# Optimization experiments

Hardware: AMD Instinct MI355X
Metric: run time of the kernel (lower is better)

Reference implementation:

```python
import jax, jax.numpy as jnp
import numpy as np

NEG_SLOPE = 0.01  # torch leaky_relu default

def _lrelu(x):
    return jax.nn.leaky_relu(x, NEG_SLOPE)

def _l2norm(x, axis):
    # torch F.normalize(p=2, eps=1e-12)
    n = jnp.linalg.norm(x, axis=axis, keepdims=True)
    return x / jnp.maximum(n, 1e-12)

def setup_inputs() -> dict:
    key = jax.random.key(0)
    ks = jax.random.split(key, 12)
    Nda, Nq, C, Din, Dout = 10000, 64, 1024, 128, 256
    target_adj = (jax.random.uniform(ks[0], (Nda, Nda)) < 0.002).astype(jnp.float32)
    query_adj = (jax.random.uniform(ks[1], (Nq, Nq)) < 0.2).astype(jnp.float32)
    node_features_da = jax.random.normal(ks[2], (Nda, Din), dtype=jnp.float32)
    node_features_q = jax.random.normal(ks[3], (Nq, Din), dtype=jnp.float32)
    candidate_set = jax.random.randint(ks[4], (C,), 0, Nda)
    candidate_adj = (jax.random.uniform(ks[5], (C, C)) < 0.01).astype(jnp.float32)
    s_in = 1.0 / np.sqrt(Din).astype(np.float32)
    s_out = 1.0 / np.sqrt(Dout).astype(np.float32)
    W1_da = jax.random.normal(ks[6], (Din, Dout), dtype=jnp.float32) * s_in
    W1_q = jax.random.normal(ks[7], (Din, Dout), dtype=jnp.float32) * s_in
    W2_da = jax.random.normal(ks[8], (Dout, Dout), dtype=jnp.float32) * s_out
    W2_q = jax.random.normal(ks[9], (Dout, Dout), dtype=jnp.float32) * s_out
    threshold = jnp.float32(0.2)
    return {"target_adj": target_adj, "node_features_da": node_features_da,
            "query_adj": query_adj, "node_features_q": node_features_q,
            "candidate_set": candidate_set, "candidate_adj": candidate_adj,
            "threshold": threshold, "W1_da": W1_da, "W1_q": W1_q,
            "W2_da": W2_da, "W2_q": W2_q}

def _cross_cosine(q, da, candidate_set):
    # cosine similarity between each query node and each candidate target node: [Nq, C]
    return _l2norm(q, 1) @ _l2norm(da[candidate_set], 1).T

def reference(target_adj, node_features_da, query_adj, node_features_q,
              candidate_set, candidate_adj, threshold, W1_da, W1_q, W2_da, W2_q):
    # layer 1: GCN propagation on both graphs (gcn(adj,x) = adj @ x @ W)
    da1 = _lrelu(target_adj @ (node_features_da @ W1_da))   # [Nda, D]
    q1 = _lrelu(query_adj @ (node_features_q @ W1_q))       # [Nq, D]
    c1 = _cross_cosine(q1, da1, candidate_set)               # [Nq, C]
    pre_da1 = da1[candidate_set]                             # [C, D]
    # NOTE: da1[candidate_set].data = ... mutates a temporary in torch -> no-op on da1
    att_da1 = _lrelu(da1)                                    # dropout in eval = identity
    h1_q = c1 @ pre_da1                                      # [Nq, D]
    att_q1 = _lrelu(q1 + _l2norm(h1_q, 0))
    # layer 2
    da2 = _lrelu(target_adj @ (att_da1 @ W2_da))
    q2 = _lrelu(query_adj @ (att_q1 @ W2_q))
    c2 = _cross_cosine(q2, da2, candidate_set)
    pre_da2 = da2[candidate_set]
    att_da2 = _lrelu(da2)                                    # in-place update is again a no-op
    h2_q = c2 @ pre_da2
    att_q2 = _lrelu(q2 + _l2norm(h2_q, 0))
    # graph-level matching score per target node
    emb = jnp.mean(att_q2, axis=0, keepdims=True)            # [1, D]
    num = att_da2 @ emb[0]                                   # [Nda]
    den = jnp.maximum(jnp.linalg.norm(att_da2, axis=1) * jnp.linalg.norm(emb), 1e-8)
    end = (num / den)[None, :]                               # [1, Nda]
    # threshold selection expressed with a mask (jit-safe, same math: excluded
    # rows/cols are zero and do not affect L2 norms, sums, or the trace)
    m = (end[0] > threshold).astype(att_da2.dtype)           # [Nda]
    F_ = att_da2 * m[:, None]
    re_adj = F_ @ F_.T                                       # [Nda, Nda]
    nor_re = _l2norm(re_adj, 1) * target_adj                 # elementwise with original adj
    cnt = jnp.sum(m)
    total = jnp.sum(nor_re)
    tr = jnp.trace(nor_re)
    has = cnt > 0
    pre_avg_degree = jnp.where(has, total / jnp.maximum(cnt, 1.0), 0.0)
    pre_avg_nodes = jnp.where(has, tr, 0.0)
    pre_density = jnp.where(has, 2.0 * total / (tr * (tr - 1.0) + 1e-4), 0.0)
    return (end, att_da2, att_q2, pre_avg_degree, pre_density, pre_avg_nodes)
```

## Files before the change

kernel.cpp:

```cpp
#include <hip/hip_runtime.h>

constexpr int NDA = 10000;
constexpr int NQ  = 64;
constexpr int CND = 1024;
constexpr int DIN = 128;
constexpr int D   = 256;
constexpr int CAP = 96;
constexpr int NB_BIG = ((NDA + 63) / 64) * (D / 64);

#define LRELU(x) ((x) >= 0.f ? (x) : 0.01f * (x))

__device__ __forceinline__ float wave_red64(float v) {
#pragma unroll
    for (int o = 32; o; o >>= 1) v += __shfl_down(v, o);
    return v;
}

struct GemmSmem { float As[32][68]; float Bs[32][68]; };

template <bool RELU_A, bool RELU_C>
__device__ __forceinline__ void gemm_body(GemmSmem& sm, int bx, int by,
                                          const float* __restrict__ A,
                                          const float* __restrict__ B,
                                          float* __restrict__ C,
                                          int M, int N, int K) {
    const int bm = bx * 64, bn = by * 64;
    const int tid = threadIdx.x;
    const int tx = tid & 15, ty = tid >> 4;
    const int lm = tid >> 2, lk = (tid & 3) * 8;
    const int kb = tid >> 3, nb = (tid & 7) * 8;
    const bool aValid = (bm + lm) < M;
    const float* aPtr = A + (size_t)(bm + lm) * K + lk;
    const float* bPtr = B + (size_t)kb * N + bn + nb;
    float4 ra0 = make_float4(0.f, 0.f, 0.f, 0.f), ra1 = ra0, rb0, rb1;
    if (aValid) { ra0 = *(const float4*)aPtr; ra1 = *(const float4*)(aPtr + 4); }
    rb0 = *(const float4*)bPtr;
    rb1 = *(const float4*)(bPtr + 4);
    float acc[4][4] = {};
    for (int k0 = 0; k0 < K; k0 += 32) {
        float4 wa0 = ra0, wa1 = ra1, wb0 = rb0, wb1 = rb1;
        if (RELU_A) {
            wa0.x = LRELU(wa0.x); wa0.y = LRELU(wa0.y); wa0.z = LRELU(wa0.z); wa0.w = LRELU(wa0.w);
            wa1.x = LRELU(wa1.x); wa1.y = LRELU(wa1.y); wa1.z = LRELU(wa1.z); wa1.w = LRELU(wa1.w);
        }
        sm.As[lk + 0][lm] = wa0.x; sm.As[lk + 1][lm] = wa0.y;
        sm.As[lk + 2][lm] = wa0.z; sm.As[lk + 3][lm] = wa0.w;
        sm.As[lk + 4][lm] = wa1.x; sm.As[lk + 5][lm] = wa1.y;
        sm.As[lk + 6][lm] = wa1.z; sm.As[lk + 7][lm] = wa1.w;
        *(float4*)&sm.Bs[kb][nb]     = wb0;
        *(float4*)&sm.Bs[kb][nb + 4] = wb1;
        __syncthreads();
        if (k0 + 32 < K) {
            if (aValid) {
                ra0 = *(const float4*)(aPtr + k0 + 32);
                ra1 = *(const float4*)(aPtr + k0 + 36);
            }
            rb0 = *(const float4*)(bPtr + (size_t)(k0 + 32) * N);
            rb1 = *(const float4*)(bPtr + (size_t)(k0 + 32) * N + 4);
        }
#pragma unroll
        for (int kk = 0; kk < 32; kk++) {
            float av[4], bv[4];
#pragma unroll
            for (int i = 0; i < 4; i++) av[i] = sm.As[kk][ty * 4 + i];
#pragma unroll
            for (int j = 0; j < 4; j++) bv[j] = sm.Bs[kk][tx * 4 + j];
#pragma unroll
            for (int i = 0; i < 4; i++)
#pragma unroll
                for (int j = 0; j < 4; j++) acc[i][j] += av[i] * bv[j];
        }
        __syncthreads();
    }
#pragma unroll
    for (int i = 0; i < 4; i++) {
        int r = bm + ty * 4 + i;
        if (r < M) {
            float4 v = make_float4(acc[i][0], acc[i][1], acc[i][2], acc[i][3]);
            if (RELU_C) { v.x = LRELU(v.x); v.y = LRELU(v.y); v.z = LRELU(v.z); v.w = LRELU(v.w); }
            *(float4*)(C + (size_t)r * N + bn + tx * 4) = v;
        }
    }
}

__device__ __forceinline__ void csr_body(const float* __restrict__ adj,
                                         int* __restrict__ cols,
                                         int* __restrict__ rowcnt, int row) {
    __shared__ int scnt;
    if (threadIdx.x == 0) scnt = 0;
    __syncthreads();
    const float4* rp = (const float4*)(adj + (size_t)row * NDA);
    for (int i = threadIdx.x; i < NDA / 4; i += 256) {
        float4 v = rp[i];
        if (v.x != 0.f) { int s = atomicAdd(&scnt, 1); if (s < CAP) cols[row * CAP + s] = 4 * i; }
        if (v.y != 0.f) { int s = atomicAdd(&scnt, 1); if (s < CAP) cols[row * CAP + s] = 4 * i + 1; }
        if (v.z != 0.f) { int s = atomicAdd(&scnt, 1); if (s < CAP) cols[row * CAP + s] = 4 * i + 2; }
        if (v.w != 0.f) { int s = atomicAdd(&scnt, 1); if (s < CAP) cols[row * CAP + s] = 4 * i + 3; }
    }
    __syncthreads();
    if (threadIdx.x == 0) rowcnt[row] = min(scnt, CAP);
}

__device__ __forceinline__ void spmm_body(const int* __restrict__ cols,
                                          const int* __restrict__ rowcnt,
                                          const float* __restrict__ X,
                                          float* __restrict__ out1,
                                          float* __restrict__ out2, int row) {
    int d = threadIdx.x;
    int cnt = rowcnt[row];
    __shared__ int sc[CAP];
    if (d < cnt) sc[d] = cols[row * CAP + d];
    __syncthreads();
    float a0 = 0.f, a1 = 0.f, a2 = 0.f, a3 = 0.f;
    int k = 0;
    for (; k + 4 <= cnt; k += 4) {
        a0 += X[(size_t)sc[k + 0] * D + d];
        a1 += X[(size_t)sc[k + 1] * D + d];
        a2 += X[(size_t)sc[k + 2] * D + d];
        a3 += X[(size_t)sc[k + 3] * D + d];
    }
    for (; k < cnt; k++) a0 += X[(size_t)sc[k] * D + d];
    float v = LRELU(a0 + a1 + a2 + a3);
    out1[(size_t)row * D + d] = v;
    if (out2) out2[(size_t)row * D + d] = LRELU(v);
}

__device__ __forceinline__ void cross_body(const float* __restrict__ q,
                                           const float* __restrict__ da,
                                           const int* __restrict__ cand,
                                           float* __restrict__ hpart,
                                           int r, int qr) {
    __shared__ float qs[D];
    __shared__ float cmw[256];
    __shared__ int sci[256];
    __shared__ float red[4];
    __shared__ float sqn;
    int d = threadIdx.x;
    float qv = q[r * D + d];
    qs[d] = qv;
    sci[d] = cand[qr * 256 + d];
    float p = wave_red64(qv * qv);
    int w = d >> 6, lane = d & 63;
    if (lane == 0) red[w] = p;
    __syncthreads();
    if (d == 0) sqn = fmaxf(sqrtf(red[0] + red[1] + red[2] + red[3]), 1e-12f);
    __syncthreads();
    float qn = sqn;
    {
        const float4* ap = (const float4*)(da + (size_t)sci[d] * D);
        float dot = 0.f, sq = 0.f;
#pragma unroll 8
        for (int k = 0; k < D / 4; k++) {
            float4 v = ap[k];
            dot += qs[4 * k] * v.x + qs[4 * k + 1] * v.y + qs[4 * k + 2] * v.z + qs[4 * k + 3] * v.w;
            sq  += v.x * v.x + v.y * v.y + v.z * v.z + v.w * v.w;
        }
        cmw[d] = dot / (qn * fmaxf(sqrtf(sq), 1e-12f));
    }
    __syncthreads();
    float a0 = 0.f, a1 = 0.f, a2 = 0.f, a3 = 0.f, a4 = 0.f, a5 = 0.f, a6 = 0.f, a7 = 0.f;
    for (int c = 0; c < 256; c += 8) {
        a0 += cmw[c + 0] * da[(size_t)sci[c + 0] * D + d];
        a1 += cmw[c + 1] * da[(size_t)sci[c + 1] * D + d];
        a2 += cmw[c + 2] * da[(size_t)sci[c + 2] * D + d];
        a3 += cmw[c + 3] * da[(size_t)sci[c + 3] * D + d];
        a4 += cmw[c + 4] * da[(size_t)sci[c + 4] * D + d];
        a5 += cmw[c + 5] * da[(size_t)sci[c + 5] * D + d];
        a6 += cmw[c + 6] * da[(size_t)sci[c + 6] * D + d];
        a7 += cmw[c + 7] * da[(size_t)sci[c + 7] * D + d];
    }
    hpart[((size_t)qr * NQ + r) * D + d] = ((a0 + a1) + (a2 + a3)) + ((a4 + a5) + (a6 + a7));
}

__global__ __launch_bounds__(256) void stage0_kernel(const float* __restrict__ adj,
                                                     int* __restrict__ cols,
                                                     int* __restrict__ rowcnt,
                                                     const float* __restrict__ Fda,
                                                     const float* __restrict__ W1da,
                                                     float* __restrict__ X1,
                                                     const float* __restrict__ Fq,
                                                     const float* __restrict__ W1q,
                                                     float* __restrict__ Xq) {
    __shared__ GemmSmem gs;
    int bid = blockIdx.x;
    if (bid < NB_BIG) {
        gemm_body<false, false>(gs, bid >> 2, bid & 3, Fda, W1da, X1, NDA, D, DIN);
    } else if (bid < NB_BIG + 4) {
        gemm_body<false, false>(gs, 0, bid - NB_BIG, Fq, W1q, Xq, NQ, D, DIN);
    } else {
        csr_body(adj, cols, rowcnt, bid - (NB_BIG + 4));
    }
}

__global__ __launch_bounds__(256) void stage_sg_kernel(const int* __restrict__ cols,
                                                       const int* __restrict__ rowcnt,
                                                       const float* __restrict__ X,
                                                       float* __restrict__ out1,
                                                       float* __restrict__ out2,
                                                       const float* __restrict__ Aq,
                                                       const float* __restrict__ Bq,
                                                       float* __restrict__ Cq) {
    __shared__ GemmSmem gs;
    int bid = blockIdx.x;
    if (bid < 4) {
        gemm_body<false, true>(gs, 0, bid, Aq, Bq, Cq, NQ, D, NQ);
    } else {
        spmm_body(cols, rowcnt, X, out1, out2, bid - 4);
    }
}

__global__ __launch_bounds__(256) void mergeA_kernel(const float* __restrict__ q1,
                                                     const float* __restrict__ da1,
                                                     const int* __restrict__ cand,
                                                     float* __restrict__ hpart,
                                                     const float* __restrict__ W2da,
                                                     float* __restrict__ Y2) {
    int bid = blockIdx.x;
    if (bid < 256) {
        cross_body(q1, da1, cand, hpart, bid >> 2, bid & 3);
    } else {
        __shared__ GemmSmem gs;
        int b = bid - 256;
        gemm_body<true, false>(gs, b >> 2, b & 3, da1, W2da, Y2, NDA, D, D);
    }
}

__global__ __launch_bounds__(256) void cross_kernel(const float* __restrict__ q,
                                                    const float* __restrict__ da,
                                                    const int* __restrict__ cand,
                                                    float* __restrict__ hpart) {
    cross_body(q, da, cand, hpart, blockIdx.x, blockIdx.y);
}

__global__ __launch_bounds__(256) void qfused_kernel(const float* __restrict__ q,
                                                     const float* __restrict__ hpart,
                                                     const float* __restrict__ W2q,
                                                     float* __restrict__ Zq) {
    __shared__ float aqT[D][68];
    __shared__ float Bs[32][68];
    int d = threadIdx.x;
    float hv[NQ];
    float ss = 0.f;
#pragma unroll
    for (int r = 0; r < NQ; r++) {
        float h = hpart[(size_t)r * D + d]
                + hpart[(size_t)(NQ + r) * D + d]
                + hpart[(size_t)(2 * NQ + r) * D + d]
                + hpart[(size_t)(3 * NQ + r) * D + d];
        hv[r] = h;
        ss += h * h;
    }
    float inv = 1.f / fmaxf(sqrtf(ss), 1e-12f);
#pragma unroll
    for (int r = 0; r < NQ; r++) {
        float v = q[r * D + d] + hv[r] * inv;
        aqT[d][r] = LRELU(v);
    }
    __syncthreads();
    const int bn = blockIdx.x * 64;
    const int tx = d & 15, ty = d >> 4;
    const int kb = d >> 3, nb = (d & 7) * 8;
    float acc[4][4] = {};
    for (int k0 = 0; k0 < D; k0 += 32) {
        float4 b0 = *(const float4*)(W2q + (size_t)(k0 + kb) * D + bn + nb);
        float4 b1 = *(const float4*)(W2q + (size_t)(k0 + kb) * D + bn + nb + 4);
        *(float4*)&Bs[kb][nb]     = b0;
        *(float4*)&Bs[kb][nb + 4] = b1;
        __syncthreads();
#pragma unroll
        for (int kk = 0; kk < 32; kk++) {
            float av[4], bv[4];
#pragma unroll
            for (int i = 0; i < 4; i++) av[i] = aqT[k0 + kk][ty * 4 + i];
#pragma unroll
            for (int j = 0; j < 4; j++) bv[j] = Bs[kk][tx * 4 + j];
#pragma unroll
            for (int i = 0; i < 4; i++)
#pragma unroll
                for (int j = 0; j < 4; j++) acc[i][j] += av[i] * bv[j];
        }
        __syncthreads();
    }
#pragma unroll
    for (int i = 0; i < 4; i++) {
        float4 v = make_float4(acc[i][0], acc[i][1], acc[i][2], acc[i][3]);
        *(float4*)(Zq + (size_t)(ty * 4 + i) * D + bn + tx * 4) = v;
    }
}

__global__ __launch_bounds__(256) void attq_kernel(const float* __restrict__ q,
                                                   const float* __restrict__ hpart,
                                                   float* __restrict__ attq,
                                                   float* __restrict__ emb) {
    int d = threadIdx.x;
    float hv[NQ];
    float ss = 0.f;
#pragma unroll
    for (int r = 0; r < NQ; r++) {
        float h = hpart[(size_t)r * D + d]
                + hpart[(size_t)(NQ + r) * D + d]
                + hpart[(size_t)(2 * NQ + r) * D + d]
                + hpart[(size_t)(3 * NQ + r) * D + d];
        hv[r] = h;
        ss += h * h;
    }
    float inv = 1.f / fmaxf(sqrtf(ss), 1e-12f);
    float es = 0.f;
#pragma unroll
    for (int r = 0; r < NQ; r++) {
        float v = q[r * D + d] + hv[r] * inv;
        v = LRELU(v);
        attq[r * D + d] = v;
        es += v;
    }
    if (emb) {
        float e = es * (1.f / (float)NQ);
        emb[d] = e;
        float p = wave_red64(e * e);
        __shared__ float red[4];
        int w = d >> 6, lane = d & 63;
        if (lane == 0) red[w] = p;
        __syncthreads();
        if (d == 0) emb[D] = sqrtf(red[0] + red[1] + red[2] + red[3]);
    }
}

__global__ __launch_bounds__(256) void end_kernel(const float* __restrict__ A,
                                                  const float* __restrict__ emb,
                                                  const float* __restrict__ thr_p,
                                                  float* __restrict__ endv,
                                                  float* __restrict__ m,
                                                  float* __restrict__ cnt) {
    __shared__ float se[D];
    __shared__ float scnt;
    int d = threadIdx.x;
    se[d] = emb[d];
    if (d == 0) scnt = 0.f;
    __syncthreads();
    float embn = emb[D];
    float thr = *thr_p;
    int w = d >> 6, lane = d & 63;
    int row = blockIdx.x * 4 + w;
    const float* ar = A + (size_t)row * D;
    float num = 0.f, sq = 0.f;
#pragma unroll
    for (int s = 0; s < 4; s++) {
        float v = ar[lane + 64 * s];
        num += v * se[lane + 64 * s];
        sq += v * v;
    }
#pragma unroll
    for (int o = 32; o; o >>= 1) { num += __shfl_down(num, o); sq += __shfl_down(sq, o); }
    if (lane == 0) {
        float den = fmaxf(sqrtf(sq) * embn, 1e-8f);
        float e = num / den;
        endv[row] = e;
        float mv = e > thr ? 1.f : 0.f;
        m[row] = mv;
        if (mv != 0.f) atomicAdd(&scnt, 1.f);
    }
    __syncthreads();
    if (d == 0 && scnt != 0.f) atomicAdd(cnt, scnt);
}

constexpr int NCHUNK = 16;
constexpr int GCHUNK = 640;
__global__ __launch_bounds__(256) void Gpart_kernel(const float* __restrict__ A,
                                                    const float* __restrict__ m,
                                                    float* __restrict__ Gp) {
    __shared__ float SA[8][64], SB[8][64];
    int ti = blockIdx.x >> 2, tj = blockIdx.x & 3;
    int base = blockIdx.y * GCHUNK;
    int tid = threadIdx.x;
    int tx = tid & 15, ty = tid >> 4;
    float acc[4][4] = {};
    for (int g0 = 0; g0 < GCHUNK; g0 += 8) {
        for (int l = tid; l < 512; l += 256) {
            int rr = l >> 6, c = l & 63;
            int r = base + g0 + rr;
            float av = 0.f, bv = 0.f, mv = 0.f;
            if (r < NDA) {
                mv = m[r];
                av = A[(size_t)r * D + ti * 64 + c];
                bv = A[(size_t)r * D + tj * 64 + c];
            }
            SA[rr][c] = av * mv;
            SB[rr][c] = bv;
        }
        __syncthreads();
#pragma unroll
        for (int rr = 0; rr < 8; rr++) {
            float av[4], bv[4];
#pragma unroll
            for (int i = 0; i < 4; i++) av[i] = SA[rr][ty * 4 + i];
#pragma unroll
            for (int j = 0; j < 4; j++) bv[j] = SB[rr][tx * 4 + j];
#pragma unroll
            for (int i = 0; i < 4; i++)
#pragma unroll
                for (int j = 0; j < 4; j++) acc[i][j] += av[i] * bv[j];
        }
        __syncthreads();
    }
    float* gp = Gp + (size_t)blockIdx.y * D * D;
#pragma unroll
    for (int i = 0; i < 4; i++)
#pragma unroll
        for (int j = 0; j < 4; j++)
            gp[(ti * 64 + ty * 4 + i) * D + tj * 64 + tx * 4 + j] = acc[i][j];
}

__global__ __launch_bounds__(256) void Gred_kernel(const float* __restrict__ Gp,
                                                   float* __restrict__ G) {
    int idx = blockIdx.x * 256 + threadIdx.x;
    float s = 0.f;
#pragma unroll
    for (int c = 0; c < NCHUNK; c++) s += Gp[(size_t)c * D * D + idx];
    G[idx] = s;
}

__global__ __launch_bounds__(256) void gemmH_kernel(const float* __restrict__ A,
                                                    const float* __restrict__ B,
                                                    float* __restrict__ C) {
    __shared__ GemmSmem gs;
    gemm_body<false, false>(gs, blockIdx.x, blockIdx.y, A, B, C, NDA, D, D);
}

__global__ __launch_bounds__(256) void final_kernel(const int* __restrict__ cols,
                                                    const int* __restrict__ rowcnt,
                                                    const float* __restrict__ m,
                                                    const float* __restrict__ A,
                                                    const float* __restrict__ H,
                                                    double* __restrict__ total,
                                                    double* __restrict__ tr) {
    int i = blockIdx.x;
    if (m[i] == 0.f) return;
    int d = threadIdx.x;
    int cnt = rowcnt[i];
    __shared__ int sc[CAP];
    __shared__ float smask[CAP];
    __shared__ int sdiag;
    __shared__ float r1[4], r2[4], r3[4];
    if (d == 0) sdiag = 0;
    if (d < cnt) {
        int j = cols[i * CAP + d];
        sc[d] = j;
        smask[d] = m[j];
        if (j == i) sdiag = 1;
    }
    __syncthreads();
    float av = A[(size_t)i * D + d];
    float hv = H[(size_t)i * D + d];
    float sd = 0.f;
    for (int k = 0; k < cnt; k++)
        if (smask[k] != 0.f) sd += A[(size_t)sc[k] * D + d];
    float p1 = av * sd, p2 = av * hv, p3 = av * av;
#pragma unroll
    for (int o = 32; o; o >>= 1) {
        p1 += __shfl_down(p1, o);
        p2 += __shfl_down(p2, o);
        p3 += __shfl_down(p3, o);
    }
    int w = d >> 6, lane = d & 63;
    if (lane == 0) { r1[w] = p1; r2[w] = p2; r3[w] = p3; }
    __syncthreads();
    if (d == 0) {
        float num  = r1[0] + r1[1] + r1[2] + r1[3];
        float den2 = r2[0] + r2[1] + r2[2] + r2[3];
        float self = r3[0] + r3[1] + r3[2] + r3[3];
        float denom = fmaxf(sqrtf(den2), 1e-12f);
        double inv = 1.0 / (double)denom;
        if (num != 0.f) atomicAdd(total, (double)num * inv);
        if (sdiag) atomicAdd(tr, (double)self * inv);
    }
}

__global__ void scalars_kernel(const float* __restrict__ cnt,
                               const double* __restrict__ total,
                               const double* __restrict__ tr,
                               float* __restrict__ out) {
    float c = *cnt;
    float T = (float)*total;
    float R = (float)*tr;
    bool has = c > 0.f;
    out[0] = has ? (T / fmaxf(c, 1.f)) : 0.f;
    out[1] = has ? (2.f * T / (R * (R - 1.f) + 1e-4f)) : 0.f;
    out[2] = has ? R : 0.f;
}

extern "C" void kernel_launch(void* const* d_in, const int* in_sizes, int n_in,
                              void* d_out, int out_size, void* d_ws, size_t ws_size,
                              hipStream_t stream) {
    (void)in_sizes; (void)n_in; (void)out_size; (void)ws_size;
    const float* adj  = (const float*)d_in[0];
    const float* Fda  = (const float*)d_in[1];
    const float* Qadj = (const float*)d_in[2];
    const float* Fq   = (const float*)d_in[3];
    const int*   cand = (const int*)d_in[4];
    const float* thr  = (const float*)d_in[6];
    const float* W1da = (const float*)d_in[7];
    const float* W1q  = (const float*)d_in[8];
    const float* W2da = (const float*)d_in[9];
    const float* W2q  = (const float*)d_in[10];

    float* out = (float*)d_out;
    float* o_end    = out;
    float* o_attda2 = out + NDA;
    float* o_attq2  = out + NDA + (size_t)NDA * D;
    float* o_sc     = o_attq2 + NQ * D;

    char* w = (char*)d_ws;
    size_t off = 0;
    auto alloc = [&](size_t b) { size_t r = off; off += (b + 255) & ~(size_t)255; return r; };
    float* bufA = (float*)(w + alloc((size_t)NDA * D * 4));
    float* bufB = (float*)(w + alloc((size_t)NDA * D * 4));
    float* bufC = (float*)(w + alloc((size_t)NDA * D * 4));
    int* colsb   = (int*)(w + alloc((size_t)NDA * CAP * 4));
    int* rowcntb = (int*)(w + alloc((size_t)NDA * 4));
    float* mbuf  = (float*)(w + alloc((size_t)NDA * 4));
    float* Gb    = (float*)(w + alloc((size_t)D * D * 4));
    float* Gp    = (float*)(w + alloc((size_t)NCHUNK * D * D * 4));
    char* zbase = w + alloc(256);
    float* cntb  = (float*)zbase;
    double* totb = (double*)(zbase + 8);
    double* trb  = (double*)(zbase + 16);
    float* xq   = (float*)(w + alloc((size_t)NQ * D * 4));
    float* q1b  = (float*)(w + alloc((size_t)NQ * D * 4));
    float* q2b  = (float*)(w + alloc((size_t)NQ * D * 4));
    float* hpart = (float*)(w + alloc((size_t)4 * NQ * D * 4));
    float* embb = (float*)(w + alloc((size_t)(D + 1) * 4));

    hipMemsetAsync(zbase, 0, 256, stream);

    stage0_kernel<<<NB_BIG + 4 + NDA, 256, 0, stream>>>(adj, colsb, rowcntb,
                                                        Fda, W1da, bufA,
                                                        Fq, W1q, xq);
    stage_sg_kernel<<<NDA + 4, 256, 0, stream>>>(colsb, rowcntb, bufA, bufB, (float*)nullptr,
                                                 Qadj, xq, q1b);
    mergeA_kernel<<<256 + NB_BIG, 256, 0, stream>>>(q1b, bufB, cand, hpart, W2da, bufA);
    qfused_kernel<<<4, 256, 0, stream>>>(q1b, hpart, W2q, xq);
    stage_sg_kernel<<<NDA + 4, 256, 0, stream>>>(colsb, rowcntb, bufA, bufC, o_attda2,
                                                 Qadj, xq, q2b);
    cross_kernel<<<dim3(NQ, 4), 256, 0, stream>>>(q2b, bufC, cand, hpart);
    attq_kernel<<<1, 256, 0, stream>>>(q2b, hpart, o_attq2, embb);
    end_kernel<<<NDA / 4, 256, 0, stream>>>(o_attda2, embb, thr, o_end, mbuf, cntb);
    Gpart_kernel<<<dim3(16, NCHUNK), 256, 0, stream>>>(o_attda2, mbuf, Gp);
    Gred_kernel<<<D * D / 256, 256, 0, stream>>>(Gp, Gb);
    gemmH_kernel<<<dim3((NDA + 63) / 64, D / 64), 256, 0, stream>>>(o_attda2, Gb, bufB);
    final_kernel<<<NDA, 256, 0, stream>>>(colsb, rowcntb, mbuf, o_attda2, bufB, totb, trb);
    scalars_kernel<<<1, 1, 0, stream>>>(cntb, totb, trb, o_sc);
}
```

Baseline: 1.060 ms.

## Use 128x128 GEMM tiles, shared-memory union, fold scalars into final kernel

Replaces the 64x64 GEMM tiles with 128x128 tiles (8x8 per thread) for the big dense GEMMs, including the Gram partials and the H product, to raise arithmetic intensity and cut shared and global traffic. Kernels now share one shared-memory union. The single-block attq kernel is split across 4 blocks, which also zero the accumulators in place of the memset. The separate scalars kernel is removed; the last block of final_kernel computes the outputs through an atomic done-counter. The larger register tile may reduce occupancy, and fewer blocks per GEMM lowers parallelism.

New measurement: 1.261 ms. 18.9% more time.

```diff
diff --git a/kernel.cpp b/kernel.cpp
--- a/kernel.cpp
+++ b/kernel.cpp
@@ -6,7 +6,10 @@
 constexpr int DIN = 128;
 constexpr int D   = 256;
 constexpr int CAP = 96;
-constexpr int NB_BIG = ((NDA + 63) / 64) * (D / 64);
+constexpr int NT128 = (NDA + 127) / 128;
+constexpr int NB128 = NT128 * 2;
+constexpr int NCHUNK = 32;
+constexpr int GCHUNK = 320;
 
 #define LRELU(x) ((x) >= 0.f ? (x) : 0.01f * (x))
 
@@ -16,7 +19,18 @@
     return v;
 }
 
-struct GemmSmem { float As[32][68]; float Bs[32][68]; };
+struct GemmSmem    { float As[32][65]; float Bs[32][68]; };
+struct Gemm128Smem { float As[16][132]; float Bs[16][132]; };
+struct CrossSmem   { float qs[D]; float cmw[256]; int sci[256]; float red[4]; float sqn; };
+struct SpmmSmem    { int sc[CAP]; };
+struct CsrSmem     { int scnt; };
+struct EndSmem     { float se[D]; float scnt; float red[4]; };
+struct FinalSmem   { int sc[CAP]; float smask[CAP]; int sdiag; float r1[4], r2[4], r3[4]; };
+struct Attq4Smem   { float hbuf[64][65]; float red[4][64]; float invs[64]; };
+union SMem {
+    GemmSmem g; Gemm128Smem h; CrossSmem c; SpmmSmem s; CsrSmem z;
+    EndSmem e; FinalSmem f; Attq4Smem a;
+};
 
 template <bool RELU_A, bool RELU_C>
 __device__ __forceinline__ void gemm_body(GemmSmem& sm, int bx, int by,
@@ -83,91 +97,149 @@
     }
 }
 
-__device__ __forceinline__ void csr_body(const float* __restrict__ adj,
+template <bool RELU_A>
+__device__ __forceinline__ void gemm128_body(Gemm128Smem& sm, int bx, int by,
+                                             const float* __restrict__ A,
+                                             const float* __restrict__ B,
+                                             float* __restrict__ C,
+                                             int M, int N, int K) {
+    const int bm = bx * 128, bn = by * 128;
+    const int tid = threadIdx.x;
+    const int tx = tid & 15, ty = tid >> 4;
+    const int am = tid >> 1, ak = (tid & 1) * 8;
+    const int bk = tid >> 4, bn8 = (tid & 15) * 8;
+    const bool aValid = (bm + am) < M;
+    const float* aPtr = A + (size_t)(bm + am) * K + ak;
+    const float* bPtr = B + (size_t)bk * N + bn + bn8;
+    float4 ra0 = make_float4(0.f, 0.f, 0.f, 0.f), ra1 = ra0, rb0, rb1;
+    if (aValid) { ra0 = *(const float4*)aPtr; ra1 = *(const float4*)(aPtr + 4); }
+    rb0 = *(const float4*)bPtr;
+    rb1 = *(const float4*)(bPtr + 4);
+    float acc[8][8] = {};
+    for (int k0 = 0; k0 < K; k0 += 16) {
+        float a8[8] = { ra0.x, ra0.y, ra0.z, ra0.w, ra1.x, ra1.y, ra1.z, ra1.w };
+        if (RELU_A) {
+#pragma unroll
+            for (int j = 0; j < 8; j++) a8[j] = LRELU(a8[j]);
+        }
+#pragma unroll
+        for (int j = 0; j < 8; j++) sm.As[ak + j][am] = a8[j];
+        *(float4*)&sm.Bs[bk][bn8]     = rb0;
+        *(float4*)&sm.Bs[bk][bn8 + 4] = rb1;
+        __syncthreads();
+        if (k0 + 16 < K) {
+            if (aValid) {
+                ra0 = *(const float4*)(aPtr + k0 + 16);
+                ra1 = *(const float4*)(aPtr + k0 + 20);
+            }
+            rb0 = *(const float4*)(bPtr + (size_t)(k0 + 16) * N);
+            rb1 = *(const float4*)(bPtr + (size_t)(k0 + 16) * N + 4);
+        }
+#pragma unroll
+        for (int kk = 0; kk < 16; kk++) {
+            float4 a0 = *(const float4*)&sm.As[kk][ty * 8];
+            float4 a1 = *(const float4*)&sm.As[kk][ty * 8 + 4];
+            float4 b0 = *(const float4*)&sm.Bs[kk][tx * 8];
+            float4 b1 = *(const float4*)&sm.Bs[kk][tx * 8 + 4];
+            float av[8] = { a0.x, a0.y, a0.z, a0.w, a1.x, a1.y, a1.z, a1.w };
+            float bv[8] = { b0.x, b0.y, b0.z, b0.w, b1.x, b1.y, b1.z, b1.w };
+#pragma unroll
+            for (int i = 0; i < 8; i++)
+#pragma unroll
+                for (int j = 0; j < 8; j++) acc[i][j] += av[i] * bv[j];
+        }
+        __syncthreads();
+    }
+#pragma unroll
+    for (int i = 0; i < 8; i++) {
+        int r = bm + ty * 8 + i;
+        if (r < M) {
+            float4 v0 = make_float4(acc[i][0], acc[i][1], acc[i][2], acc[i][3]);
+            float4 v1 = make_float4(acc[i][4], acc[i][5], acc[i][6], acc[i][7]);
+            *(float4*)(C + (size_t)r * N + bn + tx * 8)     = v0;
+            *(float4*)(C + (size_t)r * N + bn + tx * 8 + 4) = v1;
+        }
+    }
+}
+
+__device__ __forceinline__ void csr_body(CsrSmem& sm, const float* __restrict__ adj,
                                          int* __restrict__ cols,
                                          int* __restrict__ rowcnt, int row) {
-    __shared__ int scnt;
-    if (threadIdx.x == 0) scnt = 0;
+    if (threadIdx.x == 0) sm.scnt = 0;
     __syncthreads();
     const float4* rp = (const float4*)(adj + (size_t)row * NDA);
     for (int i = threadIdx.x; i < NDA / 4; i += 256) {
         float4 v = rp[i];
-        if (v.x != 0.f) { int s = atomicAdd(&scnt, 1); if (s < CAP) cols[row * CAP + s] = 4 * i; }
-        if (v.y != 0.f) { int s = atomicAdd(&scnt, 1); if (s < CAP) cols[row * CAP + s] = 4 * i + 1; }
-        if (v.z != 0.f) { int s = atomicAdd(&scnt, 1); if (s < CAP) cols[row * CAP + s] = 4 * i + 2; }
-        if (v.w != 0.f) { int s = atomicAdd(&scnt, 1); if (s < CAP) cols[row * CAP + s] = 4 * i + 3; }
-    }
-    __syncthreads();
-    if (threadIdx.x == 0) rowcnt[row] = min(scnt, CAP);
-}
-
-__device__ __forceinline__ void spmm_body(const int* __restrict__ cols,
+        if (v.x != 0.f) { int s = atomicAdd(&sm.scnt, 1); if (s < CAP) cols[row * CAP + s] = 4 * i; }
+        if (v.y != 0.f) { int s = atomicAdd(&sm.scnt, 1); if (s < CAP) cols[row * CAP + s] = 4 * i + 1; }
+        if (v.z != 0.f) { int s = atomicAdd(&sm.scnt, 1); if (s < CAP) cols[row * CAP + s] = 4 * i + 2; }
+        if (v.w != 0.f) { int s = atomicAdd(&sm.scnt, 1); if (s < CAP) cols[row * CAP + s] = 4 * i + 3; }
+    }
+    __syncthreads();
+    if (threadIdx.x == 0) rowcnt[row] = min(sm.scnt, CAP);
+}
+
+__device__ __forceinline__ void spmm_body(SpmmSmem& sm, const int* __restrict__ cols,
                                           const int* __restrict__ rowcnt,
                                           const float* __restrict__ X,
                                           float* __restrict__ out1,
                                           float* __restrict__ out2, int row) {
     int d = threadIdx.x;
     int cnt = rowcnt[row];
-    __shared__ int sc[CAP];
-    if (d < cnt) sc[d] = cols[row * CAP + d];
+    if (d < cnt) sm.sc[d] = cols[row * CAP + d];
     __syncthreads();
     float a0 = 0.f, a1 = 0.f, a2 = 0.f, a3 = 0.f;
     int k = 0;
     for (; k + 4 <= cnt; k += 4) {
-        a0 += X[(size_t)sc[k + 0] * D + d];
-        a1 += X[(size_t)sc[k + 1] * D + d];
-        a2 += X[(size_t)sc[k + 2] * D + d];
-        a3 += X[(size_t)sc[k + 3] * D + d];
-    }
-    for (; k < cnt; k++) a0 += X[(size_t)sc[k] * D + d];
+        a0 += X[(size_t)sm.sc[k + 0] * D + d];
+        a1 += X[(size_t)sm.sc[k + 1] * D + d];
+        a2 += X[(size_t)sm.sc[k + 2] * D + d];
+        a3 += X[(size_t)sm.sc[k + 3] * D + d];
+    }
+    for (; k < cnt; k++) a0 += X[(size_t)sm.sc[k] * D + d];
     float v = LRELU(a0 + a1 + a2 + a3);
     out1[(size_t)row * D + d] = v;
     if (out2) out2[(size_t)row * D + d] = LRELU(v);
 }
 
-__device__ __forceinline__ void cross_body(const float* __restrict__ q,
+__device__ __forceinline__ void cross_body(CrossSmem& sm, const float* __restrict__ q,
                                            const float* __restrict__ da,
                                            const int* __restrict__ cand,
                                            float* __restrict__ hpart,
                                            int r, int qr) {
-    __shared__ float qs[D];
-    __shared__ float cmw[256];
-    __shared__ int sci[256];
-    __shared__ float red[4];
-    __shared__ float sqn;
     int d = threadIdx.x;
     float qv = q[r * D + d];
-    qs[d] = qv;
-    sci[d] = cand[qr * 256 + d];
+    sm.qs[d] = qv;
+    sm.sci[d] = cand[qr * 256 + d];
     float p = wave_red64(qv * qv);
     int w = d >> 6, lane = d & 63;
-    if (lane == 0) red[w] = p;
-    __syncthreads();
-    if (d == 0) sqn = fmaxf(sqrtf(red[0] + red[1] + red[2] + red[3]), 1e-12f);
-    __syncthreads();
-    float qn = sqn;
+    if (lane == 0) sm.red[w] = p;
+    __syncthreads();
+    if (d == 0) sm.sqn = fmaxf(sqrtf(sm.red[0] + sm.red[1] + sm.red[2] + sm.red[3]), 1e-12f);
+    __syncthreads();
+    float qn = sm.sqn;
     {
-        const float4* ap = (const float4*)(da + (size_t)sci[d] * D);
+        const float4* ap = (const float4*)(da + (size_t)sm.sci[d] * D);
         float dot = 0.f, sq = 0.f;
 #pragma unroll 8
         for (int k = 0; k < D / 4; k++) {
             float4 v = ap[k];
-            dot += qs[4 * k] * v.x + qs[4 * k + 1] * v.y + qs[4 * k + 2] * v.z + qs[4 * k + 3] * v.w;
+            dot += sm.qs[4 * k] * v.x + sm.qs[4 * k + 1] * v.y + sm.qs[4 * k + 2] * v.z + sm.qs[4 * k + 3] * v.w;
             sq  += v.x * v.x + v.y * v.y + v.z * v.z + v.w * v.w;
         }
-        cmw[d] = dot / (qn * fmaxf(sqrtf(sq), 1e-12f));
+        sm.cmw[d] = dot / (qn * fmaxf(sqrtf(sq), 1e-12f));
     }
     __syncthreads();
     float a0 = 0.f, a1 = 0.f, a2 = 0.f, a3 = 0.f, a4 = 0.f, a5 = 0.f, a6 = 0.f, a7 = 0.f;
     for (int c = 0; c < 256; c += 8) {
-        a0 += cmw[c + 0] * da[(size_t)sci[c + 0] * D + d];
-        a1 += cmw[c + 1] * da[(size_t)sci[c + 1] * D + d];
-        a2 += cmw[c + 2] * da[(size_t)sci[c + 2] * D + d];
-        a3 += cmw[c + 3] * da[(size_t)sci[c + 3] * D + d];
-        a4 += cmw[c + 4] * da[(size_t)sci[c + 4] * D + d];
-        a5 += cmw[c + 5] * da[(size_t)sci[c + 5] * D + d];
-        a6 += cmw[c + 6] * da[(size_t)sci[c + 6] * D + d];
-        a7 += cmw[c + 7] * da[(size_t)sci[c + 7] * D + d];
+        a0 += sm.cmw[c + 0] * da[(size_t)sm.sci[c + 0] * D + d];
+        a1 += sm.cmw[c + 1] * da[(size_t)sm.sci[c + 1] * D + d];
+        a2 += sm.cmw[c + 2] * da[(size_t)sm.sci[c + 2] * D + d];
+        a3 += sm.cmw[c + 3] * da[(size_t)sm.sci[c + 3] * D + d];
+        a4 += sm.cmw[c + 4] * da[(size_t)sm.sci[c + 4] * D + d];
+        a5 += sm.cmw[c + 5] * da[(size_t)sm.sci[c + 5] * D + d];
+        a6 += sm.cmw[c + 6] * da[(size_t)sm.sci[c + 6] * D + d];
+        a7 += sm.cmw[c + 7] * da[(size_t)sm.sci[c + 7] * D + d];
     }
     hpart[((size_t)qr * NQ + r) * D + d] = ((a0 + a1) + (a2 + a3)) + ((a4 + a5) + (a6 + a7));
 }
@@ -181,14 +253,14 @@
                                                      const float* __restrict__ Fq,
                                                      const float* __restrict__ W1q,
                                                      float* __restrict__ Xq) {
-    __shared__ GemmSmem gs;
+    __shared__ SMem sm;
     int bid = blockIdx.x;
-    if (bid < NB_BIG) {
-        gemm_body<false, false>(gs, bid >> 2, bid & 3, Fda, W1da, X1, NDA, D, DIN);
-    } else if (bid < NB_BIG + 4) {
-        gemm_body<false, false>(gs, 0, bid - NB_BIG, Fq, W1q, Xq, NQ, D, DIN);
+    if (bid < NB128) {
+        gemm128_body<false>(sm.h, bid >> 1, bid & 1, Fda, W1da, X1, NDA, D, DIN);
+    } else if (bid < NB128 + 4) {
+        gemm_body<false, false>(sm.g, 0, bid - NB128, Fq, W1q, Xq, NQ, D, DIN);
     } else {
-        csr_body(adj, cols, rowcnt, bid - (NB_BIG + 4));
+        csr_body(sm.z, adj, cols, rowcnt, bid - (NB128 + 4));
     }
 }
 
@@ -200,12 +272,12 @@
                                                        const float* __restrict__ Aq,
                                                        const float* __restrict__ Bq,
                                                        float* __restrict__ Cq) {
-    __shared__ GemmSmem gs;
+    __shared__ SMem sm;
     int bid = blockIdx.x;
     if (bid < 4) {
-        gemm_body<false, true>(gs, 0, bid, Aq, Bq, Cq, NQ, D, NQ);
+        gemm_body<false, true>(sm.g, 0, bid, Aq, Bq, Cq, NQ, D, NQ);
     } else {
-        spmm_body(cols, rowcnt, X, out1, out2, bid - 4);
+        spmm_body(sm.s, cols, rowcnt, X, out1, out2, bid - 4);
     }
 }
 
@@ -215,13 +287,13 @@
                                                      float* __restrict__ hpart,
                                                      const float* __restrict__ W2da,
                                                      float* __restrict__ Y2) {
+    __shared__ SMem sm;
     int bid = blockIdx.x;
     if (bid < 256) {
-        cross_body(q1, da1, cand, hpart, bid >> 2, bid & 3);
+        cross_body(sm.c, q1, da1, cand, hpart, bid >> 2, bid & 3);
     } else {
-        __shared__ GemmSmem gs;
-        int b = bid - 256;
-        gemm_body<true, false>(gs, b >> 2, b & 3, da1, W2da, Y2, NDA, D, D);
+        int t = bid - 256;
+        gemm128_body<true>(sm.h, t >> 1, t & 1, da1, W2da, Y2, NDA, D, D);
     }
 }
 
@@ -229,14 +301,15 @@
                                                     const float* __restrict__ da,
                                                     const int* __restrict__ cand,
                                                     float* __restrict__ hpart) {
-    cross_body(q, da, cand, hpart, blockIdx.x, blockIdx.y);
+    __shared__ SMem sm;
+    cross_body(sm.c, q, da, cand, hpart, blockIdx.x, blockIdx.y);
 }
 
 __global__ __launch_bounds__(256) void qfused_kernel(const float* __restrict__ q,
                                                      const float* __restrict__ hpart,
                                                      const float* __restrict__ W2q,
                                                      float* __restrict__ Zq) {
-    __shared__ float aqT[D][68];
+    __shared__ float aqT[D][65];
     __shared__ float Bs[32][68];
     int d = threadIdx.x;
     float hv[NQ];
@@ -288,40 +361,54 @@
     }
 }
 
-__global__ __launch_bounds__(256) void attq_kernel(const float* __restrict__ q,
-                                                   const float* __restrict__ hpart,
-                                                   float* __restrict__ attq,
-                                                   float* __restrict__ emb) {
-    int d = threadIdx.x;
-    float hv[NQ];
+__global__ __launch_bounds__(256) void attq4_kernel(const float* __restrict__ q,
+                                                    const float* __restrict__ hpart,
+                                                    float* __restrict__ attq,
+                                                    float* __restrict__ emb,
+                                                    float* __restrict__ cnt,
+                                                    double* __restrict__ tot,
+                                                    double* __restrict__ tr,
+                                                    int* __restrict__ done) {
+    __shared__ SMem smu;
+    Attq4Smem& sm = smu.a;
+    int b = blockIdx.x, t = threadIdx.x;
+    int lc = t & 63, rq = t >> 6;
+    int c = b * 64 + lc;
+    if (b == 0 && t == 0) { *cnt = 0.f; *tot = 0.0; *tr = 0.0; *done = 0; }
     float ss = 0.f;
 #pragma unroll
-    for (int r = 0; r < NQ; r++) {
-        float h = hpart[(size_t)r * D + d]
-                + hpart[(size_t)(NQ + r) * D + d]
-                + hpart[(size_t)(2 * NQ + r) * D + d]
-                + hpart[(size_t)(3 * NQ + r) * D + d];
-        hv[r] = h;
+    for (int rr = 0; rr < 16; rr++) {
+        int r = rq * 16 + rr;
+        float h = hpart[(size_t)r * D + c]
+                + hpart[(size_t)(NQ + r) * D + c]
+                + hpart[(size_t)(2 * NQ + r) * D + c]
+                + hpart[(size_t)(3 * NQ + r) * D + c];
+        sm.hbuf[r][lc] = h;
         ss += h * h;
     }
-    float inv = 1.f / fmaxf(sqrtf(ss), 1e-12f);
+    sm.red[rq][lc] = ss;
+    __syncthreads();
+    if (rq == 0) {
+        float s = sm.red[0][lc] + sm.red[1][lc] + sm.red[2][lc] + sm.red[3][lc];
+        sm.invs[lc] = 1.f / fmaxf(sqrtf(s), 1e-12f);
+    }
+    __syncthreads();
+    float inv = sm.invs[lc];
     float es = 0.f;
 #pragma unroll
-    for (int r = 0; r < NQ; r++) {
-        float v = q[r * D + d] + hv[r] * inv;
+    for (int rr = 0; rr < 16; rr++) {
+        int r = rq * 16 + rr;
+        float v = q[r * D + c] + sm.hbuf[r][lc] * inv;
         v = LRELU(v);
-        attq[r * D + d] = v;
+        attq[r * D + c] = v;
         es += v;
     }
-    if (emb) {
-        float e = es * (1.f / (float)NQ);
-        emb[d] = e;
-        float p = wave_red64(e * e);
-        __shared__ float red[4];
-        int w = d >> 6, lane = d & 63;
-        if (lane == 0) red[w] = p;
-        __syncthreads();
-        if (d == 0) emb[D] = sqrtf(red[0] + red[1] + red[2] + red[3]);
+    __syncthreads();
+    sm.red[rq][lc] = es;
+    __syncthreads();
+    if (rq == 0) {
+        float e = (sm.red[0][lc] + sm.red[1][lc] + sm.red[2][lc] + sm.red[3][lc]) * (1.f / (float)NQ);
+        emb[c] = e;
     }
 }
 
@@ -331,22 +418,25 @@
                                                   float* __restrict__ endv,
                                                   float* __restrict__ m,
                                                   float* __restrict__ cnt) {
-    __shared__ float se[D];
-    __shared__ float scnt;
+    __shared__ SMem smu;
+    EndSmem& sm = smu.e;
     int d = threadIdx.x;
-    se[d] = emb[d];
-    if (d == 0) scnt = 0.f;
-    __syncthreads();
-    float embn = emb[D];
+    float ev = emb[d];
+    sm.se[d] = ev;
+    if (d == 0) sm.scnt = 0.f;
+    int w = d >> 6, lane = d & 63;
+    float pe = wave_red64(ev * ev);
+    if (lane == 0) sm.red[w] = pe;
+    __syncthreads();
+    float embn = sqrtf(sm.red[0] + sm.red[1] + sm.red[2] + sm.red[3]);
     float thr = *thr_p;
-    int w = d >> 6, lane = d & 63;
     int row = blockIdx.x * 4 + w;
     const float* ar = A + (size_t)row * D;
     float num = 0.f, sq = 0.f;
 #pragma unroll
     for (int s = 0; s < 4; s++) {
         float v = ar[lane + 64 * s];
-        num += v * se[lane + 64 * s];
+        num += v * sm.se[lane + 64 * s];
         sq += v * v;
     }
 #pragma unroll
@@ -357,57 +447,66 @@
         endv[row] = e;
         float mv = e > thr ? 1.f : 0.f;
         m[row] = mv;
-        if (mv != 0.f) atomicAdd(&scnt, 1.f);
-    }
-    __syncthreads();
-    if (d == 0 && scnt != 0.f) atomicAdd(cnt, scnt);
-}
-
-constexpr int NCHUNK = 16;
-constexpr int GCHUNK = 640;
+        if (mv != 0.f) atomicAdd(&sm.scnt, 1.f);
+    }
+    __syncthreads();
+    if (d == 0 && sm.scnt != 0.f) atomicAdd(cnt, sm.scnt);
+}
+
 __global__ __launch_bounds__(256) void Gpart_kernel(const float* __restrict__ A,
                                                     const float* __restrict__ m,
                                                     float* __restrict__ Gp) {
-    __shared__ float SA[8][64], SB[8][64];
-    int ti = blockIdx.x >> 2, tj = blockIdx.x & 3;
+    __shared__ SMem smu;
+    Gemm128Smem& sm = smu.h;
+    int ti = blockIdx.x >> 1, tj = blockIdx.x & 1;
     int base = blockIdx.y * GCHUNK;
     int tid = threadIdx.x;
     int tx = tid & 15, ty = tid >> 4;
-    float acc[4][4] = {};
-    for (int g0 = 0; g0 < GCHUNK; g0 += 8) {
-        for (int l = tid; l < 512; l += 256) {
-            int rr = l >> 6, c = l & 63;
-            int r = base + g0 + rr;
-            float av = 0.f, bv = 0.f, mv = 0.f;
-            if (r < NDA) {
-                mv = m[r];
-                av = A[(size_t)r * D + ti * 64 + c];
-                bv = A[(size_t)r * D + tj * 64 + c];
-            }
-            SA[rr][c] = av * mv;
-            SB[rr][c] = bv;
-        }
-        __syncthreads();
-#pragma unroll
-        for (int rr = 0; rr < 8; rr++) {
-            float av[4], bv[4];
-#pragma unroll
-            for (int i = 0; i < 4; i++) av[i] = SA[rr][ty * 4 + i];
-#pragma unroll
-            for (int j = 0; j < 4; j++) bv[j] = SB[rr][tx * 4 + j];
-#pragma unroll
-            for (int i = 0; i < 4; i++)
-#pragma unroll
-                for (int j = 0; j < 4; j++) acc[i][j] += av[i] * bv[j];
+    int sr = tid >> 4, sc8 = (tid & 15) * 8;
+    float acc[8][8] = {};
+    for (int g0 = 0; g0 < GCHUNK; g0 += 16) {
+        int r = base + g0 + sr;
+        float4 va0 = make_float4(0.f, 0.f, 0.f, 0.f), va1 = va0, vb0 = va0, vb1 = va0;
+        float mv = 0.f;
+        if (r < NDA) {
+            mv = m[r];
+            const float* ar = A + (size_t)r * D;
+            va0 = *(const float4*)(ar + ti * 128 + sc8);
+            va1 = *(const float4*)(ar + ti * 128 + sc8 + 4);
+            vb0 = *(const float4*)(ar + tj * 128 + sc8);
+            vb1 = *(const float4*)(ar + tj * 128 + sc8 + 4);
+        }
+        va0.x *= mv; va0.y *= mv; va0.z *= mv; va0.w *= mv;
+        va1.x *= mv; va1.y *= mv; va1.z *= mv; va1.w *= mv;
+        *(float4*)&sm.As[sr][sc8]     = va0;
+        *(float4*)&sm.As[sr][sc8 + 4] = va1;
+        *(float4*)&sm.Bs[sr][sc8]     = vb0;
+        *(float4*)&sm.Bs[sr][sc8 + 4] = vb1;
+        __syncthreads();
+#pragma unroll
+        for (int kk = 0; kk < 16; kk++) {
+            float4 a0 = *(const float4*)&sm.As[kk][ty * 8];
+            float4 a1 = *(const float4*)&sm.As[kk][ty * 8 + 4];
+            float4 b0 = *(const float4*)&sm.Bs[kk][tx * 8];
+            float4 b1 = *(const float4*)&sm.Bs[kk][tx * 8 + 4];
+            float av[8] = { a0.x, a0.y, a0.z, a0.w, a1.x, a1.y, a1.z, a1.w };
+            float bv[8] = { b0.x, b0.y, b0.z, b0.w, b1.x, b1.y, b1.z, b1.w };
+#pragma unroll
+            for (int i = 0; i < 8; i++)
+#pragma unroll
+                for (int j = 0; j < 8; j++) acc[i][j] += av[i] * bv[j];
         }
         __syncthreads();
     }
     float* gp = Gp + (size_t)blockIdx.y * D * D;
 #pragma unroll
-    for (int i = 0; i < 4; i++)
-#pragma unroll
-        for (int j = 0; j < 4; j++)
-            gp[(ti * 64 + ty * 4 + i) * D + tj * 64 + tx * 4 + j] = acc[i][j];
+    for (int i = 0; i < 8; i++) {
+        int gi = ti * 128 + ty * 8 + i;
+        float4 v0 = make_float4(acc[i][0], acc[i][1], acc[i][2], acc[i][3]);
+        float4 v1 = make_float4(acc[i][4], acc[i][5], acc[i][6], acc[i][7]);
+        *(float4*)(gp + (size_t)gi * D + tj * 128 + tx * 8)     = v0;
+        *(float4*)(gp + (size_t)gi * D + tj * 128 + tx * 8 + 4) = v1;
+    }
 }
 
 __global__ __launch_bounds__(256) void Gred_kernel(const float* __restrict__ Gp,
@@ -422,8 +521,8 @@
 __global__ __launch_bounds__(256) void gemmH_kernel(const float* __restrict__ A,
                                                     const float* __restrict__ B,
                                                     float* __restrict__ C) {
-    __shared__ GemmSmem gs;
-    gemm_body<false, false>(gs, blockIdx.x, blockIdx.y, A, B, C, NDA, D, D);
+    __shared__ SMem sm;
+    gemm128_body<false>(sm.h, blockIdx.x >> 1, blockIdx.x & 1, A, B, C, NDA, D, D);
 }
 
 __global__ __launch_bounds__(256) void final_kernel(const int* __restrict__ cols,
@@ -432,60 +531,62 @@
                                                     const float* __restrict__ A,
                                                     const float* __restrict__ H,
                                                     double* __restrict__ total,
-                                                    double* __restrict__ tr) {
+                                                    double* __restrict__ tr,
+                                                    float* __restrict__ cnt,
+                                                    int* __restrict__ done,
+                                                    float* __restrict__ o_sc) {
+    __shared__ SMem smu;
+    FinalSmem& sm = smu.f;
     int i = blockIdx.x;
-    if (m[i] == 0.f) return;
     int d = threadIdx.x;
-    int cnt = rowcnt[i];
-    __shared__ int sc[CAP];
-    __shared__ float smask[CAP];
-    __shared__ int sdiag;
-    __shared__ float r1[4], r2[4], r3[4];
-    if (d == 0) sdiag = 0;
-    if (d < cnt) {
-        int j = cols[i * CAP + d];
-        sc[d] = j;
-        smask[d] = m[j];
-        if (j == i) sdiag = 1;
-    }
-    __syncthreads();
-    float av = A[(size_t)i * D + d];
-    float hv = H[(size_t)i * D + d];
-    float sd = 0.f;
-    for (int k = 0; k < cnt; k++)
-        if (smask[k] != 0.f) sd += A[(size_t)sc[k] * D + d];
-    float p1 = av * sd, p2 = av * hv, p3 = av * av;
-#pragma unroll
-    for (int o = 32; o; o >>= 1) {
-        p1 += __shfl_down(p1, o);
-        p2 += __shfl_down(p2, o);
-        p3 += __shfl_down(p3, o);
-    }
-    int w = d >> 6, lane = d & 63;
-    if (lane == 0) { r1[w] = p1; r2[w] = p2; r3[w] = p3; }
-    __syncthreads();
+    if (m[i] != 0.f) {
+        int cnt_r = rowcnt[i];
+        if (d == 0) sm.sdiag = 0;
+        if (d < cnt_r) {
+            int j = cols[i * CAP + d];
+            sm.sc[d] = j;
+            sm.smask[d] = m[j];
+            if (j == i) sm.sdiag = 1;
+        }
+        __syncthreads();
+        float av = A[(size_t)i * D + d];
+        float hv = H[(size_t)i * D + d];
+        float sd = 0.f;
+        for (int k = 0; k < cnt_r; k++)
+            if (sm.smask[k] != 0.f) sd += A[(size_t)sm.sc[k] * D + d];
+        float p1 = av * sd, p2 = av * hv, p3 = av * av;
+#pragma unroll
+        for (int o = 32; o; o >>= 1) {
+            p1 += __shfl_down(p1, o);
+            p2 += __shfl_down(p2, o);
+            p3 += __shfl_down(p3, o);
+        }
+        int w = d >> 6, lane = d & 63;
+        if (lane == 0) { sm.r1[w] = p1; sm.r2[w] = p2; sm.r3[w] = p3; }
+        __syncthreads();
+        if (d == 0) {
+            float num  = sm.r1[0] + sm.r1[1] + sm.r1[2] + sm.r1[3];
+            float den2 = sm.r2[0] + sm.r2[1] + sm.r2[2] + sm.r2[3];
+            float self = sm.r3[0] + sm.r3[1] + sm.r3[2] + sm.r3[3];
+            float denom = fmaxf(sqrtf(den2), 1e-12f);
+            double inv = 1.0 / (double)denom;
+            if (num != 0.f) atomicAdd(total, (double)num * inv);
+            if (sm.sdiag) atomicAdd(tr, (double)self * inv);
+        }
+    }
     if (d == 0) {
-        float num  = r1[0] + r1[1] + r1[2] + r1[3];
-        float den2 = r2[0] + r2[1] + r2[2] + r2[3];
-        float self = r3[0] + r3[1] + r3[2] + r3[3];
-        float denom = fmaxf(sqrtf(den2), 1e-12f);
-        double inv = 1.0 / (double)denom;
-        if (num != 0.f) atomicAdd(total, (double)num * inv);
-        if (sdiag) atomicAdd(tr, (double)self * inv);
-    }
-}
-
-__global__ void scalars_kernel(const float* __restrict__ cnt,
-                               const double* __restrict__ total,
-                               const double* __restrict__ tr,
-                               float* __restrict__ out) {
-    float c = *cnt;
-    float T = (float)*total;
-    float R = (float)*tr;
-    bool has = c > 0.f;
-    out[0] = has ? (T / fmaxf(c, 1.f)) : 0.f;
-    out[1] = has ? (2.f * T / (R * (R - 1.f) + 1e-4f)) : 0.f;
-    out[2] = has ? R : 0.f;
+        __threadfence();
+        int prev = atomicAdd(done, 1);
+        if (prev == NDA - 1) {
+            float c = atomicAdd(cnt, 0.f);
+            float T = (float)atomicAdd(total, 0.0);
+            float R = (float)atomicAdd(tr, 0.0);
+            bool has = c > 0.f;
+            o_sc[0] = has ? (T / fmaxf(c, 1.f)) : 0.f;
+            o_sc[1] = has ? (2.f * T / (R * (R - 1.f) + 1e-4f)) : 0.f;
+            o_sc[2] = has ? R : 0.f;
+        }
+    }
 }
 
 extern "C" void kernel_launch(void* const* d_in, const int* in_sizes, int n_in,
@@ -524,29 +625,27 @@
     float* cntb  = (float*)zbase;
     double* totb = (double*)(zbase + 8);
     double* trb  = (double*)(zbase + 16);
+    int*    doneb = (int*)(zbase + 24);
     float* xq   = (float*)(w + alloc((size_t)NQ * D * 4));
     float* q1b  = (float*)(w + alloc((size_t)NQ * D * 4));
     float* q2b  = (float*)(w + alloc((size_t)NQ * D * 4));
     float* hpart = (float*)(w + alloc((size_t)4 * NQ * D * 4));
     float* embb = (float*)(w + alloc((size_t)(D + 1) * 4));
 
-    hipMemsetAsync(zbase, 0, 256, stream);
-
-    stage0_kernel<<<NB_BIG + 4 + NDA, 256, 0, stream>>>(adj, colsb, rowcntb,
-                                                        Fda, W1da, bufA,
-                                                        Fq, W1q, xq);
+    stage0_kernel<<<NB128 + 4 + NDA, 256, 0, stream>>>(adj, colsb, rowcntb,
+                                                       Fda, W1da, bufA, Fq, W1q, xq);
     stage_sg_kernel<<<NDA + 4, 256, 0, stream>>>(colsb, rowcntb, bufA, bufB, (float*)nullptr,
                                                  Qadj, xq, q1b);
-    mergeA_kernel<<<256 + NB_BIG, 256, 0, stream>>>(q1b, bufB, cand, hpart, W2da, bufA);
+    mergeA_kernel<<<256 + NB128, 256, 0, stream>>>(q1b, bufB, cand, hpart, W2da, bufA);
     qfused_kernel<<<4, 256, 0, stream>>>(q1b, hpart, W2q, xq);
     stage_sg_kernel<<<NDA + 4, 256, 0, stream>>>(colsb, rowcntb, bufA, bufC, o_attda2,
                                                  Qadj, xq, q2b);
     cross_kernel<<<dim3(NQ, 4), 256, 0, stream>>>(q2b, bufC, cand, hpart);
-    attq_kernel<<<1, 256, 0, stream>>>(q2b, hpart, o_attq2, embb);
+    attq4_kernel<<<4, 256, 0, stream>>>(q2b, hpart, o_attq2, embb, cntb, totb, trb, doneb);
     end_kernel<<<NDA / 4, 256, 0, stream>>>(o_attda2, embb, thr, o_end, mbuf, cntb);
-    Gpart_kernel<<<dim3(16, NCHUNK), 256, 0, stream>>>(o_attda2, mbuf, Gp);
+    Gpart_kernel<<<dim3(4, NCHUNK), 256, 0, stream>>>(o_attda2, mbuf, Gp);
     Gred_kernel<<<D * D / 256, 256, 0, stream>>>(Gp, Gb);
-    gemmH_kernel<<<dim3((NDA + 63) / 64, D / 64), 256, 0, stream>>>(o_attda2, Gb, bufB);
-    final_kernel<<<NDA, 256, 0, stream>>>(colsb, rowcntb, mbuf, o_attda2, bufB, totb, trb);
-    scalars_kernel<<<1, 1, 0, stream>>>(cntb, totb, trb, o_sc);
-}
+    gemmH_kernel<<<NB128, 256, 0, stream>>>(o_attda2, Gb, bufB);
+    final_kernel<<<NDA, 256, 0, stream>>>(colsb, rowcntb, mbuf, o_attda2, bufB,
+                                          totb, trb, cntb, doneb, o_sc);
+}
```
